# Optimization experiments

Measured on AMD Instinct MI355X. Metric: run time of the kernel, lower is better.

Reference implementation:

```python
import jax, jax.numpy as jnp
import numpy as np

HIDDEN = 2048
N_HEADS = 16
N_KV_HEADS = 4
HEAD_DIM = HIDDEN // N_HEADS  # 128
N_GROUPS = N_HEADS // N_KV_HEADS  # 4


def rotate_half(x):
    # interleaved rotate: (-x_odd, x_even) interleaved back
    x_even = x[..., ::2]
    x_odd = x[..., 1::2]
    return jnp.stack((-x_odd, x_even), axis=-1).reshape(x.shape)


def setup_inputs() -> dict:
    key = jax.random.key(0)
    ks = jax.random.split(key, 8)
    B, S = 4, 2048
    x = jax.random.normal(ks[0], (B, S, HIDDEN), dtype=jnp.float32)
    # RoPE tables (precomputed cos/sin over max positions)
    inv_freq = 1.0 / (1000000.0 ** (np.arange(0, HEAD_DIM, 2, dtype=np.float32) / HEAD_DIM))
    t = np.arange(S, dtype=np.float32)
    freqs = np.outer(t, inv_freq)  # [S, HEAD_DIM/2]
    emb = np.repeat(freqs, 2, axis=-1)  # interleaved layout [S, HEAD_DIM]
    cos = jnp.asarray(np.cos(emb))
    sin = jnp.asarray(np.sin(emb))
    scale = 0.02
    Wq = jax.random.normal(ks[1], (HIDDEN, N_HEADS * HEAD_DIM), dtype=jnp.float32) * scale
    Wk = jax.random.normal(ks[2], (HIDDEN, N_KV_HEADS * HEAD_DIM), dtype=jnp.float32) * scale
    Wv = jax.random.normal(ks[3], (HIDDEN, N_KV_HEADS * HEAD_DIM), dtype=jnp.float32) * scale
    Wo = jax.random.normal(ks[4], (N_HEADS * HEAD_DIM, HIDDEN), dtype=jnp.float32) * scale
    return {"x": x, "cos": cos, "sin": sin, "Wq": Wq, "Wk": Wk, "Wv": Wv, "Wo": Wo}


def reference(x, cos, sin, Wq, Wk, Wv, Wo):
    B, S, D = x.shape
    q = (x @ Wq).reshape(B, S, N_HEADS, HEAD_DIM).transpose(0, 2, 1, 3)      # [B,H,S,d]
    k = (x @ Wk).reshape(B, S, N_KV_HEADS, HEAD_DIM).transpose(0, 2, 1, 3)   # [B,Hkv,S,d]
    v = (x @ Wv).reshape(B, S, N_KV_HEADS, HEAD_DIM).transpose(0, 2, 1, 3)
    # RoPE: position_ids = arange(S); cos/sin [S,d] -> [1,1,S,d]
    c = cos[:S][None, None, :, :]
    s = sin[:S][None, None, :, :]
    q = q * c + rotate_half(q) * s
    k = k * c + rotate_half(k) * s
    # repeat_kv: [B,Hkv,S,d] -> [B,H,S,d]
    k = jnp.repeat(k, N_GROUPS, axis=1)
    v = jnp.repeat(v, N_GROUPS, axis=1)
    # causal SDPA
    scores = jnp.einsum("bhqd,bhkd->bhqk", q, k) / jnp.sqrt(jnp.float32(HEAD_DIM))
    neg = jnp.finfo(scores.dtype).min
    causal = jnp.triu(jnp.full((S, S), neg, dtype=scores.dtype), k=1)
    scores = scores + causal[None, None]
    attn = jax.nn.softmax(scores.astype(jnp.float32), axis=-1).astype(q.dtype)
    out = jnp.einsum("bhqk,bhkd->bhqd", attn, v)
    out = out.transpose(0, 2, 1, 3).reshape(B, S, N_HEADS * HEAD_DIM)
    return out @ Wo
```

## Files before the change

### kernel.cpp

```cpp
#include <hip/hip_runtime.h>
#include <stdint.h>

#define S_LEN 2048
#define BATCH 4
#define HID   2048
#define HD    128
#define NKV   4
#define KVLD  1024
#define MTOT  (BATCH*S_LEN)
#define NQT2  (S_LEN/256)
#define QSCALE 0.08838834764831845f

typedef float    f32x4  __attribute__((ext_vector_type(4)));
typedef __bf16   bf16x8 __attribute__((ext_vector_type(8)));
typedef __bf16   bf16x4 __attribute__((ext_vector_type(4)));

__device__ __forceinline__ void gld16(const void* g, void* l) {
    __builtin_amdgcn_global_load_lds(
        (const __attribute__((address_space(1))) void*)g,
        (__attribute__((address_space(3))) void*)l, 16, 0, 0);
}

__global__ void k_conv_x(const float* __restrict__ in, __bf16* __restrict__ out) {
    int i = blockIdx.x * blockDim.x + threadIdx.x;
    f32x4 a = ((const f32x4*)in)[2 * i];
    f32x4 b = ((const f32x4*)in)[2 * i + 1];
    bf16x8 o;
    o[0] = (__bf16)a[0]; o[1] = (__bf16)a[1]; o[2] = (__bf16)a[2]; o[3] = (__bf16)a[3];
    o[4] = (__bf16)b[0]; o[5] = (__bf16)b[1]; o[6] = (__bf16)b[2]; o[7] = (__bf16)b[3];
    ((bf16x8*)out)[i] = o;
}

__global__ void k_transpose_w(const float* __restrict__ in, __bf16* __restrict__ out,
                              int K, int N) {
    __shared__ float tile[64][65];
    int k0 = blockIdx.x * 64, n0 = blockIdx.y * 64;
    for (int e = threadIdx.x; e < 4096; e += 256) {
        int r = e >> 6, c = e & 63;
        tile[r][c] = in[(size_t)(k0 + r) * N + n0 + c];
    }
    __syncthreads();
    for (int e = threadIdx.x; e < 4096; e += 256) {
        int r = e >> 6, c = e & 63;
        out[(size_t)(n0 + r) * K + k0 + c] = (__bf16)tile[c][r];
    }
}

__global__ void k_transpose_v(const __bf16* __restrict__ kv, __bf16* __restrict__ vt) {
    __shared__ __bf16 tile[64][65];
    int plane = blockIdx.z;
    int b = plane >> 2, kvh = plane & 3;
    int s0 = blockIdx.x * 64, d0 = blockIdx.y * 64;
    const __bf16* src = kv + (size_t)(b * S_LEN + s0) * KVLD + NKV * HD + kvh * HD + d0;
    for (int e = threadIdx.x; e < 4096; e += 256) {
        int r = e >> 6, c = e & 63;
        tile[r][c] = src[(size_t)r * KVLD + c];
    }
    __syncthreads();
    __bf16* dst = vt + (size_t)plane * HD * S_LEN + (size_t)d0 * S_LEN + s0;
    for (int e = threadIdx.x; e < 4096; e += 256) {
        int r = e >> 6, c = e & 63;
        dst[(size_t)r * S_LEN + c] = tile[c][r];
    }
}

__global__ __launch_bounds__(256) void k_gemm_qkv(const __bf16* __restrict__ A,
                                                  const __bf16* __restrict__ Bt,
                                                  __bf16* __restrict__ qbuf,
                                                  __bf16* __restrict__ kvbuf,
                                                  const float* __restrict__ cosp,
                                                  const float* __restrict__ sinp) {
    __shared__ __align__(16) char smem[33792];
    __bf16* As = (__bf16*)smem;
    __bf16* Bs = (__bf16*)(smem + 16384);
    const int tid = threadIdx.x, lane = tid & 63, wave = tid >> 6;
    const int wm = wave >> 1, wn = wave & 1;
    const int m0 = blockIdx.x * 128, n0 = blockIdx.y * 128;
    const int lo = lane & 15, hi = lane >> 4;
    f32x4 acc[4][4] = {};

    const int srow = wave * 8 + (lane >> 3);
    const int sp   = lane & 7;

    for (int kt = 0; kt < HID; kt += 64) {
#pragma unroll
        for (int r = 0; r < 4; r++) {
            int row = r * 32 + srow;
            int c = sp ^ (row & 7);
            gld16(A + (size_t)(m0 + row) * HID + kt + c * 8, &As[(r * 32 + wave * 8) * 64]);
        }
#pragma unroll
        for (int r = 0; r < 4; r++) {
            int row = r * 32 + srow;
            int c = sp ^ (row & 7);
            gld16(Bt + (size_t)(n0 + row) * HID + kt + c * 8, &Bs[(r * 32 + wave * 8) * 64]);
        }
        __syncthreads();
#pragma unroll
        for (int ks = 0; ks < 2; ks++) {
            bf16x8 af[4], bfr[4];
#pragma unroll
            for (int mt = 0; mt < 4; mt++) {
                int row = wm * 64 + mt * 16 + lo;
                int pp = (ks * 4 + hi) ^ (row & 7);
                af[mt] = *(const bf16x8*)&As[row * 64 + pp * 8];
            }
#pragma unroll
            for (int nt = 0; nt < 4; nt++) {
                int row = wn * 64 + nt * 16 + lo;
                int pp = (ks * 4 + hi) ^ (row & 7);
                bfr[nt] = *(const bf16x8*)&Bs[row * 64 + pp * 8];
            }
#pragma unroll
            for (int mt = 0; mt < 4; mt++)
#pragma unroll
                for (int nt = 0; nt < 4; nt++)
                    acc[mt][nt] = __builtin_amdgcn_mfma_f32_16x16x32_bf16(
                        af[mt], bfr[nt], acc[mt][nt], 0, 0, 0);
        }
        __syncthreads();
    }

    __bf16* Cs = (__bf16*)smem;
#pragma unroll
    for (int mt = 0; mt < 4; mt++)
#pragma unroll
        for (int nt = 0; nt < 4; nt++) {
            int rl = wm * 64 + mt * 16 + hi * 4;
            int cl = wn * 64 + nt * 16 + lo;
#pragma unroll
            for (int r = 0; r < 4; r++)
                Cs[(rl + r) * 132 + cl] = (__bf16)acc[mt][nt][r];
        }
    __syncthreads();

    const int crow = tid >> 4;
    const int cch  = tid & 15;
    const int colg = n0 + cch * 8;
    const bool isQ = colg < 2048;
    const bool doRope = colg < 2560;
    const int d0 = colg & (HD - 1);
#pragma unroll
    for (int rep = 0; rep < 8; rep++) {
        int row = rep * 16 + crow;
        int rowg = m0 + row;
        bf16x8 v = *(const bf16x8*)&Cs[row * 132 + cch * 8];
        float f[8];
#pragma unroll
        for (int j = 0; j < 8; j++) f[j] = (float)v[j];
        if (doRope) {
            int s = rowg & (S_LEN - 1);
            f32x4 c0 = *(const f32x4*)&cosp[s * HD + d0];
            f32x4 c1 = *(const f32x4*)&cosp[s * HD + d0 + 4];
            f32x4 s0 = *(const f32x4*)&sinp[s * HD + d0];
            f32x4 s1 = *(const f32x4*)&sinp[s * HD + d0 + 4];
            float cc[8] = {c0[0], c0[1], c0[2], c0[3], c1[0], c1[1], c1[2], c1[3]};
            float ss[8] = {s0[0], s0[1], s0[2], s0[3], s1[0], s1[1], s1[2], s1[3]};
#pragma unroll
            for (int p = 0; p < 4; p++) {
                float e0 = f[2 * p], e1 = f[2 * p + 1];
                f[2 * p]     = e0 * cc[2 * p]     - e1 * ss[2 * p];
                f[2 * p + 1] = e1 * cc[2 * p + 1] + e0 * ss[2 * p + 1];
            }
            if (isQ) {
#pragma unroll
                for (int j = 0; j < 8; j++) f[j] *= QSCALE;
            }
        }
        bf16x8 o;
#pragma unroll
        for (int j = 0; j < 8; j++) o[j] = (__bf16)f[j];
        if (isQ) *(bf16x8*)&qbuf[(size_t)rowg * HID + colg] = o;
        else     *(bf16x8*)&kvbuf[(size_t)rowg * KVLD + (colg - 2048)] = o;
    }
}

template <bool OUTF32>
__global__ __launch_bounds__(256) void k_gemm(const __bf16* __restrict__ A,
                                              const __bf16* __restrict__ Bt,
                                              void* __restrict__ Cp,
                                              int M, int N, int K) {
    (void)M;
    __shared__ __bf16 As[128 * 64];
    __shared__ __bf16 Bs[128 * 64];
    const int tid = threadIdx.x, lane = tid & 63, wave = tid >> 6;
    const int wm = wave >> 1, wn = wave & 1;
    const int m0 = blockIdx.x * 128, n0 = blockIdx.y * 128;
    const int lo = lane & 15, hi = lane >> 4;
    f32x4 acc[4][4] = {};

    const int srow = wave * 8 + (lane >> 3);
    const int sp   = lane & 7;

    for (int kt = 0; kt < K; kt += 64) {
#pragma unroll
        for (int r = 0; r < 4; r++) {
            int row = r * 32 + srow;
            int c = sp ^ (row & 7);
            gld16(A + (size_t)(m0 + row) * K + kt + c * 8, &As[(r * 32 + wave * 8) * 64]);
        }
#pragma unroll
        for (int r = 0; r < 4; r++) {
            int row = r * 32 + srow;
            int c = sp ^ (row & 7);
            gld16(Bt + (size_t)(n0 + row) * K + kt + c * 8, &Bs[(r * 32 + wave * 8) * 64]);
        }
        __syncthreads();
#pragma unroll
        for (int ks = 0; ks < 2; ks++) {
            bf16x8 af[4], bfr[4];
#pragma unroll
            for (int mt = 0; mt < 4; mt++) {
                int row = wm * 64 + mt * 16 + lo;
                int pp = (ks * 4 + hi) ^ (row & 7);
                af[mt] = *(const bf16x8*)&As[row * 64 + pp * 8];
            }
#pragma unroll
            for (int nt = 0; nt < 4; nt++) {
                int row = wn * 64 + nt * 16 + lo;
                int pp = (ks * 4 + hi) ^ (row & 7);
                bfr[nt] = *(const bf16x8*)&Bs[row * 64 + pp * 8];
            }
#pragma unroll
            for (int mt = 0; mt < 4; mt++)
#pragma unroll
                for (int nt = 0; nt < 4; nt++)
                    acc[mt][nt] = __builtin_amdgcn_mfma_f32_16x16x32_bf16(
                        af[mt], bfr[nt], acc[mt][nt], 0, 0, 0);
        }
        __syncthreads();
    }
#pragma unroll
    for (int mt = 0; mt < 4; mt++) {
#pragma unroll
        for (int nt = 0; nt < 4; nt++) {
            int row = m0 + wm * 64 + mt * 16 + hi * 4;
            int col = n0 + wn * 64 + nt * 16 + lo;
#pragma unroll
            for (int r = 0; r < 4; r++) {
                if (OUTF32)
                    ((float*)Cp)[(size_t)(row + r) * N + col] = acc[mt][nt][r];
                else
                    ((__bf16*)Cp)[(size_t)(row + r) * N + col] = (__bf16)acc[mt][nt][r];
            }
        }
    }
}

__global__ __launch_bounds__(512) void k_attn(const __bf16* __restrict__ qb,
                                              const __bf16* __restrict__ kb,
                                              const __bf16* __restrict__ vtb,
                                              __bf16* __restrict__ ob) {
    __shared__ __bf16 Ks[2][64 * 128];
    __shared__ __bf16 Vs[2][128 * 64];
    __shared__ __bf16 Ps[8][2048];
    const int tid = threadIdx.x, lane = tid & 63, wave = tid >> 6;
    const int pair = blockIdx.x, h = blockIdx.y, b = blockIdx.z;
    const int kvh = h >> 2;
    const int lo = lane & 15, hi = lane >> 4;
    char* PsW = (char*)&Ps[wave][0];

    const __bf16* kbb = kb + kvh * HD + (size_t)b * S_LEN * KVLD;
    const __bf16* vbb = vtb + (size_t)(b * NKV + kvh) * HD * S_LEN;

    const int krow_s = wave * 4 + (lane >> 4);
    const int kp_s   = lane & 15;
    const int vrow_s = wave * 8 + (lane >> 3);
    const int vp_s   = lane & 7;

    auto STAGE_K = [&](int buf, int t) {
#pragma unroll
        for (int r = 0; r < 2; r++) {
            int row = r * 32 + krow_s;
            int c = kp_s ^ (row & 7);
            gld16(kbb + (size_t)(t * 64 + row) * KVLD + c * 8,
                  &Ks[buf][(r * 32 + wave * 4) * 128]);
        }
    };
    auto STAGE_V = [&](int buf, int t) {
#pragma unroll
        for (int r = 0; r < 2; r++) {
            int row = r * 64 + vrow_s;
            int c = vp_s ^ (row & 7);
            gld16(vbb + (size_t)row * S_LEN + t * 64 + c * 8,
                  &Vs[buf][(r * 64 + wave * 8) * 64]);
        }
    };

    auto SM = [&](f32x4 (&sc)[4], float& Mr, float& Lr, f32x4 (&o)[8]) {
        float mloc = sc[0][0];
#pragma unroll
        for (int nt = 0; nt < 4; nt++)
#pragma unroll
            for (int r = 0; r < 4; r++) mloc = fmaxf(mloc, sc[nt][r]);
        mloc = fmaxf(mloc, __shfl_xor(mloc, 16, 64));
        mloc = fmaxf(mloc, __shfl_xor(mloc, 32, 64));
        float mn = (mloc <= Mr + 8.f) ? Mr : mloc;
        float sum = 0.f;
#pragma unroll
        for (int nt = 0; nt < 4; nt++)
#pragma unroll
            for (int r = 0; r < 4; r++) {
                float e = __expf(sc[nt][r] - mn);
                sc[nt][r] = e;
                sum += e;
            }
        sum += __shfl_xor(sum, 16, 64);
        sum += __shfl_xor(sum, 32, 64);
        if (mn != Mr) {
            float scl = __expf(Mr - mn);
            Lr = Lr * scl + sum;
            Mr = mn;
#pragma unroll
            for (int dt = 0; dt < 8; dt++) o[dt] *= scl;
        } else {
            Lr += sum;
        }
    };

#pragma unroll 1
    for (int pi = 0; pi < 2; pi++) {
        const int qt = pi ? (NQT2 - 1 - pair) : pair;
        const int nkv = 4 * qt + 4;
        const int qbase = qt * 256 + wave * 32;

        const __bf16* qptr0 = qb + (size_t)(b * S_LEN + qbase + lo) * HID + h * HD;
        const __bf16* qptr1 = qptr0 + (size_t)16 * HID;
        bf16x8 qa0[4], qa1[4];
#pragma unroll
        for (int kf = 0; kf < 4; kf++) {
            qa0[kf] = *(const bf16x8*)(qptr0 + kf * 32 + hi * 8);
            qa1[kf] = *(const bf16x8*)(qptr1 + kf * 32 + hi * 8);
        }

        f32x4 o0[8] = {}, o1[8] = {};
        float Mr0 = -3e30f, Lr0 = 0.f, Mr1 = -3e30f, Lr1 = 0.f;

        int cur = 0;
        if (pi == 1) __syncthreads();
        STAGE_K(0, 0);
        STAGE_V(0, 0);
        __syncthreads();

#pragma unroll 1
        for (int t = 0; t < nkv; t++) {
            if (t < nkv - 1) { STAGE_K(cur ^ 1, t + 1); STAGE_V(cur ^ 1, t + 1); }

            f32x4 sc0[4], sc1[4];
            __builtin_amdgcn_s_setprio(1);
#pragma unroll
            for (int nt = 0; nt < 4; nt++) {
                f32x4 a = {0.f, 0.f, 0.f, 0.f}, bb = {0.f, 0.f, 0.f, 0.f};
#pragma unroll
                for (int kf = 0; kf < 4; kf++) {
                    int row = nt * 16 + lo;
                    int pp = (kf * 4 + hi) ^ (row & 7);
                    bf16x8 kf8 = *(const bf16x8*)&Ks[cur][row * 128 + pp * 8];
                    a  = __builtin_amdgcn_mfma_f32_16x16x32_bf16(kf8, qa0[kf], a, 0, 0, 0);
                    bb = __builtin_amdgcn_mfma_f32_16x16x32_bf16(kf8, qa1[kf], bb, 0, 0, 0);
                }
                sc0[nt] = a; sc1[nt] = bb;
            }
            __builtin_amdgcn_s_setprio(0);

            if (t * 64 + 63 > qbase) {
                int qg = qbase + lo;
#pragma unroll
                for (int nt = 0; nt < 4; nt++)
#pragma unroll
                    for (int r = 0; r < 4; r++) {
                        int kg = t * 64 + nt * 16 + hi * 4 + r;
                        if (kg > qg) sc0[nt][r] = -1e30f;
                    }
            }
            if (t * 64 + 63 > qbase + 16) {
                int qg = qbase + 16 + lo;
#pragma unroll
                for (int nt = 0; nt < 4; nt++)
#pragma unroll
                    for (int r = 0; r < 4; r++) {
                        int kg = t * 64 + nt * 16 + hi * 4 + r;
                        if (kg > qg) sc1[nt][r] = -1e30f;
                    }
            }

            SM(sc0, Mr0, Lr0, o0);
            SM(sc1, Mr1, Lr1, o1);

#pragma unroll
            for (int nt = 0; nt < 4; nt++) {
                bf16x4 p0, p1;
#pragma unroll
                for (int r = 0; r < 4; r++) { p0[r] = (__bf16)sc0[nt][r]; p1[r] = (__bf16)sc1[nt][r]; }
                int off = lo * 128 + ((nt * 32 + hi * 8) ^ ((lo & 7) << 4));
                *(bf16x4*)(PsW + off)        = p0;
                *(bf16x4*)(PsW + 2048 + off) = p1;
            }
            asm volatile("s_waitcnt lgkmcnt(0)" ::: "memory");
            bf16x8 pf0[2], pf1[2];
#pragma unroll
            for (int c = 0; c < 2; c++) {
                int off = lo * 128 + ((c * 64 + hi * 16) ^ ((lo & 7) << 4));
                pf0[c] = *(const bf16x8*)(PsW + off);
                pf1[c] = *(const bf16x8*)(PsW + 2048 + off);
            }
            __builtin_amdgcn_s_setprio(1);
#pragma unroll
            for (int dt = 0; dt < 8; dt++) {
                int rowd = dt * 16 + lo;
#pragma unroll
                for (int c = 0; c < 2; c++) {
                    int ch = c * 4 + hi;
                    bf16x8 vv = *(const bf16x8*)&Vs[cur][rowd * 64 + (ch ^ (rowd & 7)) * 8];
                    o0[dt] = __builtin_amdgcn_mfma_f32_16x16x32_bf16(vv, pf0[c], o0[dt], 0, 0, 0);
                    o1[dt] = __builtin_amdgcn_mfma_f32_16x16x32_bf16(vv, pf1[c], o1[dt], 0, 0, 0);
                }
            }
            __builtin_amdgcn_s_setprio(0);
            __syncthreads();
            cur ^= 1;
        }

        const int qe = lane >> 2, c4 = lane & 3;
#pragma unroll
        for (int sub = 0; sub < 2; sub++) {
            float rl = 1.0f / (sub ? Lr1 : Lr0);
            char* Pp = PsW + sub * 2048;
#pragma unroll
            for (int h2 = 0; h2 < 2; h2++) {
#pragma unroll
                for (int dt4 = 0; dt4 < 4; dt4++) {
                    f32x4 ov = sub ? o1[h2 * 4 + dt4] : o0[h2 * 4 + dt4];
                    bf16x4 w;
#pragma unroll
                    for (int r = 0; r < 4; r++) w[r] = (__bf16)(ov[r] * rl);
                    *(bf16x4*)(Pp + lo * 128 + ((dt4 * 32 + hi * 8) ^ ((lo & 7) << 4))) = w;
                }
                asm volatile("s_waitcnt lgkmcnt(0)" ::: "memory");
                __builtin_amdgcn_sched_barrier(0);
#pragma unroll
                for (int s2 = 0; s2 < 2; s2++) {
                    int ch = c4 + s2 * 4;
                    bf16x8 v = *(const bf16x8*)(Pp + qe * 128 + ((ch * 16) ^ ((qe & 7) << 4)));
                    int qg = qbase + sub * 16 + qe;
                    int col = h * HD + h2 * 64 + ch * 8;
                    *(bf16x8*)&ob[(size_t)(b * S_LEN + qg) * HID + col] = v;
                }
            }
        }
    }
}

extern "C" void kernel_launch(void* const* d_in, const int* in_sizes, int n_in,
                              void* d_out, int out_size, void* d_ws, size_t ws_size,
                              hipStream_t stream) {
    (void)in_sizes; (void)n_in; (void)out_size; (void)ws_size;
    const float* x    = (const float*)d_in[0];
    const float* cosp = (const float*)d_in[1];
    const float* sinp = (const float*)d_in[2];
    const float* Wq   = (const float*)d_in[3];
    const float* Wk   = (const float*)d_in[4];
    const float* Wv   = (const float*)d_in[5];
    const float* Wo   = (const float*)d_in[6];
    float* out = (float*)d_out;

    char* ws = (char*)d_ws;
    __bf16* xb   = (__bf16*)(ws);
    __bf16* wqt  = (__bf16*)(ws + 33554432);
    __bf16* wkvt = (__bf16*)(ws + 41943040);
    __bf16* wot  = (__bf16*)(ws + 46137344);
    __bf16* qbuf = (__bf16*)(ws + 54525952);
    __bf16* kv   = (__bf16*)(ws + 88080384);
    __bf16* vtb  = (__bf16*)(ws + 104857600);
    __bf16* aob  = xb;

    k_conv_x<<<MTOT * HID / 8 / 256, 256, 0, stream>>>(x, xb);
    { dim3 g(32, 32); k_transpose_w<<<g, 256, 0, stream>>>(Wq, wqt, HID, HID); }
    { dim3 g(32, 8);  k_transpose_w<<<g, 256, 0, stream>>>(Wk, wkvt, HID, NKV * HD); }
    { dim3 g(32, 8);  k_transpose_w<<<g, 256, 0, stream>>>(Wv, wkvt + (size_t)512 * HID, HID, NKV * HD); }
    { dim3 g(32, 32); k_transpose_w<<<g, 256, 0, stream>>>(Wo, wot, HID, HID); }

    { dim3 g(MTOT / 128, 3072 / 128);
      k_gemm_qkv<<<g, 256, 0, stream>>>(xb, wqt, qbuf, kv, cosp, sinp); }

    { dim3 g(S_LEN / 64, HD / 64, 16); k_transpose_v<<<g, 256, 0, stream>>>(kv, vtb); }
    { dim3 g(NQT2 / 2, 16, BATCH);     k_attn<<<g, 512, 0, stream>>>(qbuf, kv, vtb, aob); }

    { dim3 g(MTOT / 128, HID / 128);
      k_gemm<true><<<g, 256, 0, stream>>>(aob, wot, out, MTOT, HID, HID); }
}
```

Measured before the change: 357.8 us.

## Store Q/K as FP8 for FP8 QK^T MFMA and fuse V transpose into QKV GEMM

The QKV GEMM epilogue now quantizes RoPE'd Q and K to FP8 e4m3 and writes V directly in transposed layout, which removes the separate V-transpose kernel. The attention kernel stages K as FP8, halving the K tile size, and computes scores with fp8 MFMA instead of bf16. This cuts Q/K memory traffic and one launch, and may speed up the QK product. In exchange, Q and K lose precision, which can affect attention accuracy.

```diff
diff --git a/kernel.cpp b/kernel.cpp
--- a/kernel.cpp
+++ b/kernel.cpp
@@ -6,7 +6,6 @@
 #define HID   2048
 #define HD    128
 #define NKV   4
-#define KVLD  1024
 #define MTOT  (BATCH*S_LEN)
 #define NQT2  (S_LEN/256)
 #define QSCALE 0.08838834764831845f
@@ -14,6 +13,7 @@
 typedef float    f32x4  __attribute__((ext_vector_type(4)));
 typedef __bf16   bf16x8 __attribute__((ext_vector_type(8)));
 typedef __bf16   bf16x4 __attribute__((ext_vector_type(4)));
+typedef unsigned u32x2  __attribute__((ext_vector_type(2)));
 
 __device__ __forceinline__ void gld16(const void* g, void* l) {
     __builtin_amdgcn_global_load_lds(
@@ -46,28 +46,11 @@
     }
 }
 
-__global__ void k_transpose_v(const __bf16* __restrict__ kv, __bf16* __restrict__ vt) {
-    __shared__ __bf16 tile[64][65];
-    int plane = blockIdx.z;
-    int b = plane >> 2, kvh = plane & 3;
-    int s0 = blockIdx.x * 64, d0 = blockIdx.y * 64;
-    const __bf16* src = kv + (size_t)(b * S_LEN + s0) * KVLD + NKV * HD + kvh * HD + d0;
-    for (int e = threadIdx.x; e < 4096; e += 256) {
-        int r = e >> 6, c = e & 63;
-        tile[r][c] = src[(size_t)r * KVLD + c];
-    }
-    __syncthreads();
-    __bf16* dst = vt + (size_t)plane * HD * S_LEN + (size_t)d0 * S_LEN + s0;
-    for (int e = threadIdx.x; e < 4096; e += 256) {
-        int r = e >> 6, c = e & 63;
-        dst[(size_t)r * S_LEN + c] = tile[c][r];
-    }
-}
-
 __global__ __launch_bounds__(256) void k_gemm_qkv(const __bf16* __restrict__ A,
                                                   const __bf16* __restrict__ Bt,
-                                                  __bf16* __restrict__ qbuf,
-                                                  __bf16* __restrict__ kvbuf,
+                                                  unsigned char* __restrict__ qb8,
+                                                  unsigned char* __restrict__ kb8,
+                                                  __bf16* __restrict__ vtb,
                                                   const float* __restrict__ cosp,
                                                   const float* __restrict__ sinp) {
     __shared__ __align__(16) char smem[33792];
@@ -121,57 +104,87 @@
         __syncthreads();
     }
 
-    __bf16* Cs = (__bf16*)smem;
-#pragma unroll
-    for (int mt = 0; mt < 4; mt++)
-#pragma unroll
-        for (int nt = 0; nt < 4; nt++) {
-            int rl = wm * 64 + mt * 16 + hi * 4;
-            int cl = wn * 64 + nt * 16 + lo;
-#pragma unroll
-            for (int r = 0; r < 4; r++)
-                Cs[(rl + r) * 132 + cl] = (__bf16)acc[mt][nt][r];
-        }
-    __syncthreads();
-
-    const int crow = tid >> 4;
-    const int cch  = tid & 15;
-    const int colg = n0 + cch * 8;
-    const bool isQ = colg < 2048;
-    const bool doRope = colg < 2560;
-    const int d0 = colg & (HD - 1);
-#pragma unroll
-    for (int rep = 0; rep < 8; rep++) {
-        int row = rep * 16 + crow;
-        int rowg = m0 + row;
-        bf16x8 v = *(const bf16x8*)&Cs[row * 132 + cch * 8];
-        float f[8];
-#pragma unroll
-        for (int j = 0; j < 8; j++) f[j] = (float)v[j];
-        if (doRope) {
-            int s = rowg & (S_LEN - 1);
-            f32x4 c0 = *(const f32x4*)&cosp[s * HD + d0];
-            f32x4 c1 = *(const f32x4*)&cosp[s * HD + d0 + 4];
-            f32x4 s0 = *(const f32x4*)&sinp[s * HD + d0];
-            f32x4 s1 = *(const f32x4*)&sinp[s * HD + d0 + 4];
-            float cc[8] = {c0[0], c0[1], c0[2], c0[3], c1[0], c1[1], c1[2], c1[3]};
-            float ss[8] = {s0[0], s0[1], s0[2], s0[3], s1[0], s1[1], s1[2], s1[3]};
-#pragma unroll
-            for (int p = 0; p < 4; p++) {
-                float e0 = f[2 * p], e1 = f[2 * p + 1];
-                f[2 * p]     = e0 * cc[2 * p]     - e1 * ss[2 * p];
-                f[2 * p + 1] = e1 * cc[2 * p + 1] + e0 * ss[2 * p + 1];
+    if (n0 < 2560) {
+        __bf16* Cs = (__bf16*)smem;
+#pragma unroll
+        for (int mt = 0; mt < 4; mt++)
+#pragma unroll
+            for (int nt = 0; nt < 4; nt++) {
+                int rl = wm * 64 + mt * 16 + hi * 4;
+                int cl = wn * 64 + nt * 16 + lo;
+#pragma unroll
+                for (int r = 0; r < 4; r++)
+                    Cs[(rl + r) * 132 + cl] = (__bf16)acc[mt][nt][r];
+            }
+        __syncthreads();
+
+        const int crow = tid >> 4;
+        const int cch  = tid & 15;
+        const int colg = n0 + cch * 8;
+        const bool isQ = n0 < 2048;
+        const int d0 = colg & (HD - 1);
+#pragma unroll
+        for (int rep = 0; rep < 8; rep++) {
+            int row = rep * 16 + crow;
+            int rowg = m0 + row;
+            bf16x8 v = *(const bf16x8*)&Cs[row * 132 + cch * 8];
+            float f[8];
+#pragma unroll
+            for (int j = 0; j < 8; j++) f[j] = (float)v[j];
+            {
+                int s = rowg & (S_LEN - 1);
+                f32x4 c0 = *(const f32x4*)&cosp[s * HD + d0];
+                f32x4 c1 = *(const f32x4*)&cosp[s * HD + d0 + 4];
+                f32x4 s0 = *(const f32x4*)&sinp[s * HD + d0];
+                f32x4 s1 = *(const f32x4*)&sinp[s * HD + d0 + 4];
+                float cc[8] = {c0[0], c0[1], c0[2], c0[3], c1[0], c1[1], c1[2], c1[3]};
+                float ss[8] = {s0[0], s0[1], s0[2], s0[3], s1[0], s1[1], s1[2], s1[3]};
+#pragma unroll
+                for (int p = 0; p < 4; p++) {
+                    float e0 = f[2 * p], e1 = f[2 * p + 1];
+                    f[2 * p]     = e0 * cc[2 * p]     - e1 * ss[2 * p];
+                    f[2 * p + 1] = e1 * cc[2 * p + 1] + e0 * ss[2 * p + 1];
+                }
             }
             if (isQ) {
 #pragma unroll
                 for (int j = 0; j < 8; j++) f[j] *= QSCALE;
             }
-        }
-        bf16x8 o;
-#pragma unroll
-        for (int j = 0; j < 8; j++) o[j] = (__bf16)f[j];
-        if (isQ) *(bf16x8*)&qbuf[(size_t)rowg * HID + colg] = o;
-        else     *(bf16x8*)&kvbuf[(size_t)rowg * KVLD + (colg - 2048)] = o;
+            int u0 = __builtin_amdgcn_cvt_pk_fp8_f32(f[0], f[1], 0, false);
+            u0     = __builtin_amdgcn_cvt_pk_fp8_f32(f[2], f[3], u0, true);
+            int u1 = __builtin_amdgcn_cvt_pk_fp8_f32(f[4], f[5], 0, false);
+            u1     = __builtin_amdgcn_cvt_pk_fp8_f32(f[6], f[7], u1, true);
+            u32x2 pk; pk[0] = (unsigned)u0; pk[1] = (unsigned)u1;
+            if (isQ) *(u32x2*)&qb8[(size_t)rowg * HID + colg] = pk;
+            else     *(u32x2*)&kb8[(size_t)rowg * 512 + (colg - 2048)] = pk;
+        }
+    } else {
+        __bf16* CsT = (__bf16*)smem;
+#pragma unroll
+        for (int mt = 0; mt < 4; mt++)
+#pragma unroll
+            for (int nt = 0; nt < 4; nt++) {
+                int cl = wn * 64 + nt * 16 + lo;
+                int mrow = wm * 64 + mt * 16 + hi * 4;
+                bf16x4 w;
+#pragma unroll
+                for (int r = 0; r < 4; r++) w[r] = (__bf16)acc[mt][nt][r];
+                *(bf16x4*)&CsT[cl * 132 + mrow] = w;
+            }
+        __syncthreads();
+
+        const int kvh = (n0 - 2560) >> 7;
+        const int bb = m0 >> 11;
+        const int s0 = m0 & (S_LEN - 1);
+        __bf16* dst = vtb + (size_t)(bb * NKV + kvh) * HD * S_LEN;
+        const int dloc = tid >> 4;
+        const int sch  = tid & 15;
+#pragma unroll
+        for (int rep = 0; rep < 8; rep++) {
+            int d = rep * 16 + dloc;
+            bf16x8 v = *(const bf16x8*)&CsT[d * 132 + sch * 8];
+            *(bf16x8*)&dst[(size_t)d * S_LEN + s0 + sch * 8] = v;
+        }
     }
 }
 
@@ -247,11 +260,11 @@
     }
 }
 
-__global__ __launch_bounds__(512) void k_attn(const __bf16* __restrict__ qb,
-                                              const __bf16* __restrict__ kb,
+__global__ __launch_bounds__(512) void k_attn(const unsigned char* __restrict__ qb8,
+                                              const unsigned char* __restrict__ kb8,
                                               const __bf16* __restrict__ vtb,
                                               __bf16* __restrict__ ob) {
-    __shared__ __bf16 Ks[2][64 * 128];
+    __shared__ char   Ks8[2][64 * 128];
     __shared__ __bf16 Vs[2][128 * 64];
     __shared__ __bf16 Ps[8][2048];
     const int tid = threadIdx.x, lane = tid & 63, wave = tid >> 6;
@@ -260,22 +273,18 @@
     const int lo = lane & 15, hi = lane >> 4;
     char* PsW = (char*)&Ps[wave][0];
 
-    const __bf16* kbb = kb + kvh * HD + (size_t)b * S_LEN * KVLD;
+    const unsigned char* kbb = kb8 + (size_t)b * S_LEN * 512 + kvh * HD;
     const __bf16* vbb = vtb + (size_t)(b * NKV + kvh) * HD * S_LEN;
 
-    const int krow_s = wave * 4 + (lane >> 4);
-    const int kp_s   = lane & 15;
+    const int krow_s = tid >> 3;
+    const int kp_s   = tid & 7;
     const int vrow_s = wave * 8 + (lane >> 3);
     const int vp_s   = lane & 7;
 
     auto STAGE_K = [&](int buf, int t) {
-#pragma unroll
-        for (int r = 0; r < 2; r++) {
-            int row = r * 32 + krow_s;
-            int c = kp_s ^ (row & 7);
-            gld16(kbb + (size_t)(t * 64 + row) * KVLD + c * 8,
-                  &Ks[buf][(r * 32 + wave * 4) * 128]);
-        }
+        int c = kp_s ^ (krow_s & 7);
+        gld16(kbb + (size_t)(t * 64 + krow_s) * 512 + c * 16,
+              &Ks8[buf][wave * 1024]);
     };
     auto STAGE_V = [&](int buf, int t) {
 #pragma unroll
@@ -324,13 +333,13 @@
         const int nkv = 4 * qt + 4;
         const int qbase = qt * 256 + wave * 32;
 
-        const __bf16* qptr0 = qb + (size_t)(b * S_LEN + qbase + lo) * HID + h * HD;
-        const __bf16* qptr1 = qptr0 + (size_t)16 * HID;
-        bf16x8 qa0[4], qa1[4];
+        const unsigned char* qp0 = qb8 + (size_t)(b * S_LEN + qbase + lo) * HID + h * HD;
+        const unsigned char* qp1 = qp0 + (size_t)16 * HID;
+        long qa0[4], qa1[4];
 #pragma unroll
         for (int kf = 0; kf < 4; kf++) {
-            qa0[kf] = *(const bf16x8*)(qptr0 + kf * 32 + hi * 8);
-            qa1[kf] = *(const bf16x8*)(qptr1 + kf * 32 + hi * 8);
+            qa0[kf] = *(const long*)(qp0 + kf * 32 + hi * 8);
+            qa1[kf] = *(const long*)(qp1 + kf * 32 + hi * 8);
         }
 
         f32x4 o0[8] = {}, o1[8] = {};
@@ -354,10 +363,11 @@
 #pragma unroll
                 for (int kf = 0; kf < 4; kf++) {
                     int row = nt * 16 + lo;
-                    int pp = (kf * 4 + hi) ^ (row & 7);
-                    bf16x8 kf8 = *(const bf16x8*)&Ks[cur][row * 128 + pp * 8];
-                    a  = __builtin_amdgcn_mfma_f32_16x16x32_bf16(kf8, qa0[kf], a, 0, 0, 0);
-                    bb = __builtin_amdgcn_mfma_f32_16x16x32_bf16(kf8, qa1[kf], bb, 0, 0, 0);
+                    int lch = 2 * kf + (hi >> 1);
+                    long kf8 = *(const long*)&Ks8[cur][row * 128 +
+                                ((lch ^ (row & 7)) * 16) + (hi & 1) * 8];
+                    a  = __builtin_amdgcn_mfma_f32_16x16x32_fp8_fp8(kf8, qa0[kf], a, 0, 0, 0);
+                    bb = __builtin_amdgcn_mfma_f32_16x16x32_fp8_fp8(kf8, qa1[kf], bb, 0, 0, 0);
                 }
                 sc0[nt] = a; sc1[nt] = bb;
             }
@@ -465,14 +475,14 @@
     float* out = (float*)d_out;
 
     char* ws = (char*)d_ws;
-    __bf16* xb   = (__bf16*)(ws);
-    __bf16* wqt  = (__bf16*)(ws + 33554432);
-    __bf16* wkvt = (__bf16*)(ws + 41943040);
-    __bf16* wot  = (__bf16*)(ws + 46137344);
-    __bf16* qbuf = (__bf16*)(ws + 54525952);
-    __bf16* kv   = (__bf16*)(ws + 88080384);
-    __bf16* vtb  = (__bf16*)(ws + 104857600);
-    __bf16* aob  = xb;
+    __bf16*        xb   = (__bf16*)(ws);
+    __bf16*        wqt  = (__bf16*)(ws + 33554432);
+    __bf16*        wkvt = (__bf16*)(ws + 41943040);
+    __bf16*        wot  = (__bf16*)(ws + 46137344);
+    unsigned char* qb8  = (unsigned char*)(ws + 54525952);
+    unsigned char* kb8  = (unsigned char*)(ws + 71303168);
+    __bf16*        vtb  = (__bf16*)(ws + 75497472);
+    __bf16*        aob  = xb;
 
     k_conv_x<<<MTOT * HID / 8 / 256, 256, 0, stream>>>(x, xb);
     { dim3 g(32, 32); k_transpose_w<<<g, 256, 0, stream>>>(Wq, wqt, HID, HID); }
@@ -481,10 +491,9 @@
     { dim3 g(32, 32); k_transpose_w<<<g, 256, 0, stream>>>(Wo, wot, HID, HID); }
 
     { dim3 g(MTOT / 128, 3072 / 128);
-      k_gemm_qkv<<<g, 256, 0, stream>>>(xb, wqt, qbuf, kv, cosp, sinp); }
-
-    { dim3 g(S_LEN / 64, HD / 64, 16); k_transpose_v<<<g, 256, 0, stream>>>(kv, vtb); }
-    { dim3 g(NQT2 / 2, 16, BATCH);     k_attn<<<g, 512, 0, stream>>>(qbuf, kv, vtb, aob); }
+      k_gemm_qkv<<<g, 256, 0, stream>>>(xb, wqt, qb8, kb8, vtb, cosp, sinp); }
+
+    { dim3 g(NQT2 / 2, 16, BATCH); k_attn<<<g, 512, 0, stream>>>(qb8, kb8, vtb, aob); }
 
     { dim3 g(MTOT / 128, HID / 128);
       k_gemm<true><<<g, 256, 0, stream>>>(aob, wot, out, MTOT, HID, HID); }
```

New measurement: 345.7 us. -3.4%, faster.
